# Performance work log

Measured on AMD Instinct MI355X. Metric: run time of the kernel, lower is better.

Reference implementation:

```python
import jax, jax.numpy as jnp
import numpy as np

B, S, HID = 2, 1024, 4096
NH, NKV, HD = 32, 8, 128
GROUPS = NH // NKV  # 4
BITS = 8
SCALING = HD ** -0.5


def quantize_lastdim(x, bits=BITS):
    """Asymmetric min-max fake-quant per row of the last dim (groupsize=-1),
    matching ActQuantizer.find_params + quantize/dequantize."""
    qmax = float(2 ** bits - 1)
    xmin = jnp.minimum(jnp.min(x, axis=-1, keepdims=True), 0.0)
    xmax = jnp.maximum(jnp.max(x, axis=-1, keepdims=True), 0.0)
    rng = xmax - xmin
    scale = jnp.where(rng == 0, 1.0, rng / qmax)
    zero = jnp.round(-xmin / scale)
    q = jnp.clip(jnp.round(x / scale) + zero, 0.0, qmax)
    return (q - zero) * scale


def rotate_half(x):
    x1, x2 = jnp.split(x, 2, axis=-1)
    return jnp.concatenate([-x2, x1], axis=-1)


def setup_inputs() -> dict:
    key = jax.random.key(0)
    ks = jax.random.split(key, 5)
    hidden_states = jax.random.normal(ks[0], (B, S, HID), dtype=jnp.float32)
    w_std = 0.02
    Wq = w_std * jax.random.normal(ks[1], (NH * HD, HID), dtype=jnp.float32)
    Wk = w_std * jax.random.normal(ks[2], (NKV * HD, HID), dtype=jnp.float32)
    Wv = w_std * jax.random.normal(ks[3], (NKV * HD, HID), dtype=jnp.float32)
    Wo = w_std * jax.random.normal(ks[4], (HID, NH * HD), dtype=jnp.float32)
    # RoPE tables (theta=10000)
    inv_freq = 1.0 / (10000.0 ** (jnp.arange(0, HD, 2, dtype=jnp.float32) / HD))
    freqs = jnp.outer(jnp.arange(S, dtype=jnp.float32), inv_freq)  # [S, HD/2]
    emb = jnp.concatenate([freqs, freqs], axis=-1)  # [S, HD]
    cos = jnp.broadcast_to(jnp.cos(emb)[None], (B, S, HD)).astype(jnp.float32)
    sin = jnp.broadcast_to(jnp.sin(emb)[None], (B, S, HD)).astype(jnp.float32)
    # additive causal mask [B,1,S,S]
    causal = jnp.tril(jnp.ones((S, S), dtype=bool))
    attention_mask = jnp.where(causal, 0.0, -1e9).astype(jnp.float32)
    attention_mask = jnp.broadcast_to(attention_mask[None, None], (B, 1, S, S))
    return {"hidden_states": hidden_states, "cos": cos, "sin": sin,
            "attention_mask": attention_mask, "Wq": Wq, "Wk": Wk, "Wv": Wv, "Wo": Wo}


def reference(hidden_states, cos, sin, attention_mask, Wq, Wk, Wv, Wo):
    b, s, _ = hidden_states.shape
    # projections -> [B, H, S, D]
    q = (hidden_states @ Wq.T).reshape(b, s, NH, HD).transpose(0, 2, 1, 3)
    k = (hidden_states @ Wk.T).reshape(b, s, NKV, HD).transpose(0, 2, 1, 3)
    v = (hidden_states @ Wv.T).reshape(b, s, NKV, HD).transpose(0, 2, 1, 3)
    # RoPE (HF: unsqueeze cos/sin at head dim)
    c = cos[:, None, :, :]
    si = sin[:, None, :, :]
    q = q * c + rotate_half(q) * si
    k = k * c + rotate_half(k) * si
    # SmoothK per-channel: subtract per-channel mean over the sequence
    # (softmax-invariant outlier smoothing of K before quantization)
    k = k - jnp.mean(k, axis=2, keepdims=True)
    # activation fake-quant of Q, K (per token over head_dim)
    q = quantize_lastdim(q)
    k = quantize_lastdim(k)
    # V quantized along the sequence axis (module transposes dims 2,3 first)
    v = quantize_lastdim(v.transpose(0, 1, 3, 2)).transpose(0, 1, 3, 2)
    # GQA repeat
    k_rep = jnp.repeat(k, GROUPS, axis=1)
    v_rep = jnp.repeat(v, GROUPS, axis=1)
    scores = jnp.einsum('bhqd,bhkd->bhqk', q, k_rep) * SCALING + attention_mask
    w = jax.nn.softmax(scores.astype(jnp.float32), axis=-1).astype(q.dtype)
    # fake-quant attention weights per row (groupsize=-1, so no padding)
    w = quantize_lastdim(w)
    attn = jnp.einsum('bhqk,bhkd->bhqd', w, v_rep)
    attn = attn.transpose(0, 2, 1, 3).reshape(b, s, NH * HD)
    out = attn @ Wo.T
    return (out, w)
```

## Files before the change

kernel.cpp:

```cpp
#include <hip/hip_runtime.h>
#include <math.h>
#include <stdint.h>

typedef unsigned int u32;
typedef unsigned short u16;
typedef __bf16 bf16x8 __attribute__((ext_vector_type(8)));
typedef float f32x4 __attribute__((ext_vector_type(4)));
typedef unsigned short u16x8 __attribute__((ext_vector_type(8)));
typedef unsigned short u16x4 __attribute__((ext_vector_type(4)));

constexpr int   Bb  = 2;
constexpr int   Ss  = 1024;
constexpr int   HID = 4096;
constexpr int   NH  = 32;
constexpr int   NKV = 8;
constexpr int   HD  = 128;
constexpr float SCALING = 0.0883883476483184405501f;

enum { M_QKV = 0, M_OUT = 3 };

__device__ __forceinline__ u16 f2bf(float f) {
  u32 u = __builtin_bit_cast(u32, f);
  u = u + 0x7fffu + ((u >> 16) & 1u);
  return (u16)(u >> 16);
}

__device__ __forceinline__ void gld_lds16(const void* g, void* l) {
  __builtin_amdgcn_global_load_lds(
      (const __attribute__((address_space(1))) u32*)(uintptr_t)g,
      (__attribute__((address_space(3))) u32*)(uintptr_t)l, 16, 0, 0);
}

template <int MODE>
__global__ __launch_bounds__(512) void mfma_gemm(
    const u16* __restrict__ Abf_g,
    const u16* __restrict__ B0, const u16* __restrict__ B1,
    const u16* __restrict__ B2,
    float* __restrict__ Cf, float* __restrict__ Ck, float* __restrict__ Cv,
    int K) {
  __shared__ u16 As[3][128 * 64];
  __shared__ u16 Bs[3][256 * 64];

  const int tid = threadIdx.x;
  const int lane = tid & 63;
  const int wid = tid >> 6;
  const int wr = wid >> 2;
  const int wc = wid & 3;
  const int fr = lane & 15;
  const int fq = lane >> 4;

  constexpr int GX = (MODE == M_QKV) ? 24 : 16;
  constexpr int CPX = (MODE == M_QKV) ? 48 : 32;
  const int bid = blockIdx.x;
  const int wg = (bid & 7) * CPX + (bid >> 3);
  const int bx = wg % GX;
  const int by = wg / GX;

  const int m0 = by * 128;
  int nloc = 0;

  const u16* Abf = Abf_g + (size_t)m0 * K;
  const u16* Bp = nullptr;
  int which = 0;

  if (MODE == M_QKV) {
    if (bx < 16)      { which = 0; Bp = B0 + (size_t)bx * 256 * K;        nloc = bx * 256; }
    else if (bx < 20) { which = 1; Bp = B1 + (size_t)(bx - 16) * 256 * K; nloc = (bx - 16) * 256; }
    else              { which = 2; Bp = B2 + (size_t)(bx - 20) * 256 * K; nloc = (bx - 20) * 256; }
  } else {
    Bp = B0 + (size_t)bx * 256 * K;
    nloc = bx * 256;
  }

  f32x4 acc[4][4];
#pragma unroll
  for (int i = 0; i < 4; i++)
#pragma unroll
    for (int j = 0; j < 4; j++) acc[i][j] = (f32x4){0.f, 0.f, 0.f, 0.f};

  const int arow0 = wr * 64 + wc * 16;
  const int brow0 = wc * 64 + wr * 32;
  const int sub8 = lane >> 3;
  const int sl8 = lane & 7;

  auto stageA = [&](int t, int s) {
    const int ko = t * 64;
#pragma unroll
    for (int g = 0; g < 2; ++g) {
      const int r0 = arow0 + g * 8;
      const int row = r0 + sub8;
      gld_lds16(Abf + (size_t)row * K + ko + ((sl8 ^ (row & 7)) * 8),
                &As[s][r0 * 64]);
    }
  };
  auto stageB2 = [&](int t, int s, int gbase) {
    const int ko = t * 64;
#pragma unroll
    for (int g = 0; g < 2; ++g) {
      const int r0 = brow0 + (gbase + g) * 8;
      const int row = r0 + sub8;
      gld_lds16(Bp + (size_t)row * K + ko + ((sl8 ^ (row & 7)) * 8),
                &Bs[s][r0 * 64]);
    }
  };

  const int nk = K >> 6;

  stageA(0, 0); stageB2(0, 0, 0); stageB2(0, 0, 2);
  stageA(1, 1); stageB2(1, 1, 0); stageB2(1, 1, 2);
  asm volatile("s_waitcnt vmcnt(6)" ::: "memory");
  __builtin_amdgcn_sched_barrier(0);
  __builtin_amdgcn_s_barrier();

  int buf = 0, nxt = 2;
  for (int kt = 0; kt < nk; ++kt) {
    const bool st = (kt + 2 < nk);

    {
      bf16x8 av[4], bv[4];
#pragma unroll
      for (int i = 0; i < 4; ++i) {
        const int r = wr * 64 + i * 16 + fr;
        av[i] = *(const bf16x8*)&As[buf][r * 64 + ((fq ^ (r & 7)) * 8)];
      }
#pragma unroll
      for (int j = 0; j < 4; ++j) {
        const int r = wc * 64 + j * 16 + fr;
        bv[j] = *(const bf16x8*)&Bs[buf][r * 64 + ((fq ^ (r & 7)) * 8)];
      }
      if (st) { stageA(kt + 2, nxt); stageB2(kt + 2, nxt, 0); }
      __builtin_amdgcn_s_barrier();
      asm volatile("s_waitcnt lgkmcnt(0)" ::: "memory");
      __builtin_amdgcn_sched_barrier(0);
      __builtin_amdgcn_s_setprio(1);
#pragma unroll
      for (int i = 0; i < 4; i++)
#pragma unroll
        for (int j = 0; j < 4; j++)
          acc[i][j] = __builtin_amdgcn_mfma_f32_16x16x32_bf16(av[i], bv[j], acc[i][j], 0, 0, 0);
      __builtin_amdgcn_s_setprio(0);
    }

    {
      bf16x8 av[4], bv[4];
#pragma unroll
      for (int i = 0; i < 4; ++i) {
        const int r = wr * 64 + i * 16 + fr;
        av[i] = *(const bf16x8*)&As[buf][r * 64 + (((4 + fq) ^ (r & 7)) * 8)];
      }
#pragma unroll
      for (int j = 0; j < 4; ++j) {
        const int r = wc * 64 + j * 16 + fr;
        bv[j] = *(const bf16x8*)&Bs[buf][r * 64 + (((4 + fq) ^ (r & 7)) * 8)];
      }
      if (st) { stageB2(kt + 2, nxt, 2); }
      __builtin_amdgcn_s_barrier();
      asm volatile("s_waitcnt lgkmcnt(0)" ::: "memory");
      __builtin_amdgcn_sched_barrier(0);
      __builtin_amdgcn_s_setprio(1);
#pragma unroll
      for (int i = 0; i < 4; i++)
#pragma unroll
        for (int j = 0; j < 4; j++)
          acc[i][j] = __builtin_amdgcn_mfma_f32_16x16x32_bf16(av[i], bv[j], acc[i][j], 0, 0, 0);
      __builtin_amdgcn_s_setprio(0);
    }

    if (st) {
      asm volatile("s_waitcnt vmcnt(6)" ::: "memory");
    } else {
      asm volatile("s_waitcnt vmcnt(0)" ::: "memory");
    }
    __builtin_amdgcn_sched_barrier(0);
    __builtin_amdgcn_s_barrier();
    buf = (buf == 2) ? 0 : buf + 1;
    nxt = (nxt == 2) ? 0 : nxt + 1;
  }

#pragma unroll
  for (int i = 0; i < 4; i++) {
#pragma unroll
    for (int j = 0; j < 4; j++) {
      const int n = nloc + wc * 64 + j * 16 + fr;
      const int mb = m0 + wr * 64 + i * 16 + fq * 4;
      if (MODE == M_QKV && which == 2) {
        const int b = mb >> 10, s = mb & 1023, h = n >> 7, d = n & 127;
        float4 v4 = {acc[i][j][0], acc[i][j][1], acc[i][j][2], acc[i][j][3]};
        *(float4*)&Cv[((size_t)(b * NKV + h) * HD + d) * Ss + s] = v4;
      } else {
#pragma unroll
        for (int e = 0; e < 4; e++) {
          const int m = mb + e;
          float val = acc[i][j][e];
          if (MODE == M_QKV) {
            const int b = m >> 10, s = m & 1023, h = n >> 7, d = n & 127;
            if (which == 0) Cf[((size_t)(b * NH + h) * Ss + s) * HD + d] = val;
            else            Ck[((size_t)(b * NKV + h) * Ss + s) * HD + d] = val;
          } else {
            Cf[(size_t)m * HID + n] = val;
          }
        }
      }
    }
  }
}

__global__ __launch_bounds__(512, 4) void fused_attn(
    const u16* __restrict__ qb,
    const u16* __restrict__ kb,
    const u16* __restrict__ vTb,
    float* __restrict__ wout,
    u16* __restrict__ attnb) {
  __shared__ u16 Ks[2][64 * 128];
  __shared__ u16 Vs[2][128 * 64];
  __shared__ float scl_l[8][16];

  const int a = 7 - (int)(blockIdx.x >> 6);
  const int bh = blockIdx.x & 63;
  const int b = bh >> 5, h = bh & 31;
  const int kv = h >> 2;
  const int tid = threadIdx.x;
  const int lane = tid & 63;
  const int wq = tid >> 6;
  const int fr = lane & 15, fq = lane >> 4;

  const int nt = 2 * a + 2;
  const int Q0 = a * 128;
  const int qw0 = Q0 + wq * 16;
  const int dband = qw0 >> 6;

  const u16* Kb = kb + (size_t)(b * NKV + kv) * Ss * HD;
  const u16* Vb = vTb + (size_t)(b * NKV + kv) * HD * Ss;
  float* wrow = wout + (size_t)bh * Ss * Ss;

  if (a < 7) {
    const int base = 64 * nt;
    const int n4 = (Ss - base) >> 2;
    const int row = Q0 + (tid >> 2);
    float4* wp = (float4*)&wrow[(size_t)row * Ss + base];
    for (int c = tid & 3; c < n4; c += 4) wp[c] = float4{0.f, 0.f, 0.f, 0.f};
  }

  auto stageK = [&](int t, int s) {
#pragma unroll
    for (int g = 0; g < 2; ++g) {
      const int c = wq * 2 + g;
      const int idx = c * 64 + lane;
      const int row = idx >> 4, sl = idx & 15;
      const int slot = sl ^ (row & 15);
      gld_lds16(Kb + (size_t)(t * 64 + row) * HD + slot * 8, &Ks[s][c * 512]);
    }
  };
  auto stageV = [&](int t, int s) {
#pragma unroll
    for (int g = 0; g < 2; ++g) {
      const int c = wq * 2 + g;
      const int idx = c * 64 + lane;
      const int d = idx >> 3, sl = idx & 7;
      const int slot = sl ^ (d & 7);
      gld_lds16(Vb + (size_t)d * Ss + t * 64 + slot * 8, &Vs[s][c * 512]);
    }
  };

  bf16x8 qf[4];
#pragma unroll
  for (int kk = 0; kk < 4; kk++)
    qf[kk] = *(const bf16x8*)&qb[((size_t)bh * Ss + qw0 + fr) * HD + kk * 32 + fq * 8];

  float m[4], l[4];
#pragma unroll
  for (int i = 0; i < 4; i++) { m[i] = -1e30f; l[i] = 0.f; }

  stageK(0, 0);
  for (int t = 0; t < nt; ++t) {
    if (t + 1 < nt) {
      stageK(t + 1, (t + 1) & 1);
      asm volatile("s_waitcnt vmcnt(2)" ::: "memory");
    } else {
      asm volatile("s_waitcnt vmcnt(0)" ::: "memory");
    }
    __builtin_amdgcn_sched_barrier(0);
    __builtin_amdgcn_s_barrier();
    const u16* Kt = &Ks[t & 1][0];

    f32x4 sa[4];
#pragma unroll
    for (int jn = 0; jn < 4; jn++) sa[jn] = (f32x4){0.f, 0.f, 0.f, 0.f};
#pragma unroll
    for (int kk = 0; kk < 4; ++kk) {
      bf16x8 kfv[4];
#pragma unroll
      for (int jn = 0; jn < 4; ++jn) {
        const int row = jn * 16 + fr;
        kfv[jn] = *(const bf16x8*)&Kt[row * 128 + (((kk * 4 + fq) ^ fr) * 8)];
      }
#pragma unroll
      for (int jn = 0; jn < 4; ++jn)
        sa[jn] = __builtin_amdgcn_mfma_f32_16x16x32_bf16(qf[kk], kfv[jn], sa[jn], 0, 0, 0);
    }

    const bool diag = (t >= dband);
#pragma unroll
    for (int e = 0; e < 4; ++e) {
      const int qrow = qw0 + fq * 4 + e;
      float sv[4];
      float rmax = -1e30f;
#pragma unroll
      for (int jn = 0; jn < 4; ++jn) {
        float s = sa[jn][e] * SCALING;
        if (diag && (t * 64 + jn * 16 + fr > qrow)) s = -1e30f;
        sv[jn] = s;
        rmax = fmaxf(rmax, s);
      }
#pragma unroll
      for (int o = 1; o < 16; o <<= 1) rmax = fmaxf(rmax, __shfl_xor(rmax, o));
      const float mn = fmaxf(m[e], rmax);
      const float cc = __expf(m[e] - mn);
      float rs = __expf(sv[0] - mn) + __expf(sv[1] - mn) +
                 __expf(sv[2] - mn) + __expf(sv[3] - mn);
#pragma unroll
      for (int o = 1; o < 16; o <<= 1) rs += __shfl_xor(rs, o);
      l[e] = l[e] * cc + rs;
      m[e] = mn;
    }
    __builtin_amdgcn_s_barrier();
  }

  float scl[4];
#pragma unroll
  for (int e = 0; e < 4; e++) scl[e] = 1.f / (255.f * l[e]);
  if (fr == 0) {
#pragma unroll
    for (int e = 0; e < 4; e++) scl_l[wq][fq * 4 + e] = scl[e];
  }

  f32x4 acc2[8];
#pragma unroll
  for (int j = 0; j < 8; j++) acc2[j] = (f32x4){0.f, 0.f, 0.f, 0.f};

  const int wrrow = lane >> 2, wrq = lane & 3;
  const float sclr = scl_l[wq][wrrow];

  stageK(0, 0);
  stageV(0, 0);
  for (int t = 0; t < nt; ++t) {
    if (t + 1 < nt) {
      stageK(t + 1, (t + 1) & 1);
      stageV(t + 1, (t + 1) & 1);
      asm volatile("s_waitcnt vmcnt(4)" ::: "memory");
    } else {
      asm volatile("s_waitcnt vmcnt(0)" ::: "memory");
    }
    __builtin_amdgcn_sched_barrier(0);
    __builtin_amdgcn_s_barrier();
    const u16* Kt = &Ks[t & 1][0];
    const u16* Vt = &Vs[t & 1][0];
    u16* pl = &Ks[t & 1][wq * 1024];

    f32x4 sa[4];
#pragma unroll
    for (int jn = 0; jn < 4; jn++) sa[jn] = (f32x4){0.f, 0.f, 0.f, 0.f};
#pragma unroll
    for (int kk = 0; kk < 4; ++kk) {
      bf16x8 kfv[4];
#pragma unroll
      for (int jn = 0; jn < 4; ++jn) {
        const int row = jn * 16 + fr;
        kfv[jn] = *(const bf16x8*)&Kt[row * 128 + (((kk * 4 + fq) ^ fr) * 8)];
      }
#pragma unroll
      for (int jn = 0; jn < 4; ++jn)
        sa[jn] = __builtin_amdgcn_mfma_f32_16x16x32_bf16(qf[kk], kfv[jn], sa[jn], 0, 0, 0);
    }
    __builtin_amdgcn_s_barrier();

    const bool diag = (t >= dband);
#pragma unroll
    for (int e = 0; e < 4; ++e) {
      const int qrow = qw0 + fq * 4 + e;
      const int r16 = fq * 4 + e;
#pragma unroll
      for (int jn = 0; jn < 4; ++jn) {
        const int kc = t * 64 + jn * 16 + fr;
        float qv = 0.f;
        if (!diag || kc <= qrow)
          qv = rintf(fminf(255.f * __expf(sa[jn][e] * SCALING - m[e]), 255.f));
        const int col = jn * 16 + fr;
        const int byte = r16 * 128 + (((col >> 3) ^ (r16 & 7)) * 16) + (col & 7) * 2;
        *(u16*)((char*)pl + byte) = f2bf(qv);
      }
    }

    {
      const int s0 = (2 * wrq) ^ (wrrow & 7);
      const int s1 = (2 * wrq + 1) ^ (wrrow & 7);
      bf16x8 p0 = *(const bf16x8*)((char*)pl + wrrow * 128 + s0 * 16);
      bf16x8 p1 = *(const bf16x8*)((char*)pl + wrrow * 128 + s1 * 16);
      float* wp = &wrow[(size_t)(qw0 + wrrow) * Ss + t * 64 + wrq * 16];
      float4 o0, o1, o2, o3;
      o0.x = (float)p0[0] * sclr; o0.y = (float)p0[1] * sclr;
      o0.z = (float)p0[2] * sclr; o0.w = (float)p0[3] * sclr;
      o1.x = (float)p0[4] * sclr; o1.y = (float)p0[5] * sclr;
      o1.z = (float)p0[6] * sclr; o1.w = (float)p0[7] * sclr;
      o2.x = (float)p1[0] * sclr; o2.y = (float)p1[1] * sclr;
      o2.z = (float)p1[2] * sclr; o2.w = (float)p1[3] * sclr;
      o3.x = (float)p1[4] * sclr; o3.y = (float)p1[5] * sclr;
      o3.z = (float)p1[6] * sclr; o3.w = (float)p1[7] * sclr;
      ((float4*)wp)[0] = o0; ((float4*)wp)[1] = o1;
      ((float4*)wp)[2] = o2; ((float4*)wp)[3] = o3;
    }

#pragma unroll
    for (int kk2 = 0; kk2 < 2; ++kk2) {
      const bf16x8 pa = *(const bf16x8*)((char*)pl + fr * 128 + (((kk2 * 4 + fq) ^ (fr & 7)) * 16));
#pragma unroll
      for (int jn2 = 0; jn2 < 8; ++jn2) {
        const int d = jn2 * 16 + fr;
        const bf16x8 vb = *(const bf16x8*)&Vt[d * 64 + (((kk2 * 4 + fq) ^ (d & 7)) * 8)];
        acc2[jn2] = __builtin_amdgcn_mfma_f32_16x16x32_bf16(pa, vb, acc2[jn2], 0, 0, 0);
      }
    }
    __builtin_amdgcn_s_barrier();
  }

#pragma unroll
  for (int e = 0; e < 4; ++e) {
    const int qrow = qw0 + fq * 4 + e;
#pragma unroll
    for (int jn2 = 0; jn2 < 8; ++jn2)
      attnb[((size_t)b * Ss + qrow) * HID + h * HD + jn2 * 16 + fr] =
          f2bf(acc2[jn2][e] * scl[e]);
  }
}

constexpr int CB_HS = Bb * Ss * HID / 2048;
constexpr int CB_WQ = NH * HD * HID / 2048;
constexpr int CB_WK = NKV * HD * HID / 2048;
constexpr int CB_WV = CB_WK;
constexpr int CB_WO = HID * NH * HD / 2048;

__global__ __launch_bounds__(256) void convert_all(
    const float* __restrict__ hs, const float* __restrict__ wq,
    const float* __restrict__ wk, const float* __restrict__ wv,
    const float* __restrict__ wo,
    u16* __restrict__ hsb, u16* __restrict__ wqb, u16* __restrict__ wkb,
    u16* __restrict__ wvb, u16* __restrict__ wob) {
  const int bid = blockIdx.x;
  const float* src;
  u16* dst;
  int base;
  if (bid < CB_HS) { src = hs; dst = hsb; base = 0; }
  else if (bid < CB_HS + CB_WQ) { src = wq; dst = wqb; base = CB_HS; }
  else if (bid < CB_HS + CB_WQ + CB_WK) { src = wk; dst = wkb; base = CB_HS + CB_WQ; }
  else if (bid < CB_HS + CB_WQ + CB_WK + CB_WV) { src = wv; dst = wvb; base = CB_HS + CB_WQ + CB_WK; }
  else { src = wo; dst = wob; base = CB_HS + CB_WQ + CB_WK + CB_WV; }
  const int i = (bid - base) * 256 + threadIdx.x;
  float4 a = ((const float4*)src)[2 * i];
  float4 b = ((const float4*)src)[2 * i + 1];
  u16x8 t;
  t[0] = f2bf(a.x); t[1] = f2bf(a.y); t[2] = f2bf(a.z); t[3] = f2bf(a.w);
  t[4] = f2bf(b.x); t[5] = f2bf(b.y); t[6] = f2bf(b.z); t[7] = f2bf(b.w);
  ((u16x8*)dst)[i] = t;
}

constexpr int PQ_Q = (Bb * NH * Ss) / 4;
constexpr int PQ_K = (Bb * NKV * Ss) / 4;
constexpr int PQ_V = Bb * NKV * HD;

__global__ __launch_bounds__(256) void postq(
    const float* __restrict__ q, u16* __restrict__ qb,
    float* __restrict__ k,
    const float* __restrict__ vT, u16* __restrict__ vTb,
    const float* __restrict__ cs, const float* __restrict__ sn) {
  const int bid = blockIdx.x;
  if (bid < PQ_Q) {
    const int row = bid * 4 + (threadIdx.x >> 6);
    const int lane = threadIdx.x & 63;
    const int s = row & (Ss - 1);
    const int b = row >> 15;
    const float* p = q + (size_t)row * HD;
    const float* cp = cs + ((size_t)b * Ss + s) * HD;
    const float* sp = sn + ((size_t)b * Ss + s) * HD;
    float x1 = p[lane], x2 = p[lane + 64];
    float r1 = x1 * cp[lane] - x2 * sp[lane];
    float r2 = x2 * cp[lane + 64] + x1 * sp[lane + 64];
    float mn = fminf(0.f, fminf(r1, r2));
    float mx = fmaxf(0.f, fmaxf(r1, r2));
#pragma unroll
    for (int o = 32; o; o >>= 1) {
      mn = fminf(mn, __shfl_xor(mn, o));
      mx = fmaxf(mx, __shfl_xor(mx, o));
    }
    float rng = mx - mn;
    float scale = (rng == 0.f) ? 1.f : rng / 255.f;
    float zero = rintf(-mn / scale);
    float q1 = fminf(fmaxf(rintf(r1 / scale) + zero, 0.f), 255.f);
    float q2 = fminf(fmaxf(rintf(r2 / scale) + zero, 0.f), 255.f);
    qb[(size_t)row * HD + lane] = f2bf((q1 - zero) * scale);
    qb[(size_t)row * HD + lane + 64] = f2bf((q2 - zero) * scale);
  } else if (bid < PQ_Q + PQ_K) {
    const int row = (bid - PQ_Q) * 4 + (threadIdx.x >> 6);
    const int lane = threadIdx.x & 63;
    const int s = row & (Ss - 1);
    const int b = row >> 13;
    float* p = k + (size_t)row * HD;
    const float* cp = cs + ((size_t)b * Ss + s) * HD;
    const float* sp = sn + ((size_t)b * Ss + s) * HD;
    float x1 = p[lane], x2 = p[lane + 64];
    float r1 = x1 * cp[lane] - x2 * sp[lane];
    float r2 = x2 * cp[lane + 64] + x1 * sp[lane + 64];
    p[lane] = r1;
    p[lane + 64] = r2;
  } else {
    const int vb = bid - PQ_Q - PQ_K;
    const float* p = vT + (size_t)vb * Ss;
    const int t = threadIdx.x;
    float4 x = ((const float4*)p)[t];
    float mn = fminf(0.f, fminf(fminf(x.x, x.y), fminf(x.z, x.w)));
    float mx = fmaxf(0.f, fmaxf(fmaxf(x.x, x.y), fmaxf(x.z, x.w)));
#pragma unroll
    for (int o = 32; o; o >>= 1) {
      mn = fminf(mn, __shfl_xor(mn, o));
      mx = fmaxf(mx, __shfl_xor(mx, o));
    }
    __shared__ float smn[4], smx[4];
    const int wid = t >> 6, lane = t & 63;
    if (lane == 0) { smn[wid] = mn; smx[wid] = mx; }
    __syncthreads();
    mn = fminf(fminf(smn[0], smn[1]), fminf(smn[2], smn[3]));
    mx = fmaxf(fmaxf(smx[0], smx[1]), fmaxf(smx[2], smx[3]));
    float rng = mx - mn;
    float scale = (rng == 0.f) ? 1.f : rng / 255.f;
    float zero = rintf(-mn / scale);
    u16x4 o4;
    o4[0] = f2bf((fminf(fmaxf(rintf(x.x / scale) + zero, 0.f), 255.f) - zero) * scale);
    o4[1] = f2bf((fminf(fmaxf(rintf(x.y / scale) + zero, 0.f), 255.f) - zero) * scale);
    o4[2] = f2bf((fminf(fmaxf(rintf(x.z / scale) + zero, 0.f), 255.f) - zero) * scale);
    o4[3] = f2bf((fminf(fmaxf(rintf(x.w / scale) + zero, 0.f), 255.f) - zero) * scale);
    ((u16x4*)vTb)[(size_t)vb * 256 + t] = o4;
  }
}

__global__ __launch_bounds__(1024) void kmean_kernel(const float* __restrict__ k,
                                                     float* __restrict__ kmean) {
  const int bh = blockIdx.x;
  const int d = threadIdx.x & 127;
  const int sl = threadIdx.x >> 7;
  const float* p = k + (size_t)bh * Ss * HD;
  float sum = 0.f;
  for (int s = sl; s < Ss; s += 8) sum += p[(size_t)s * HD + d];
  __shared__ float lds[8][128];
  lds[sl][d] = sum;
  __syncthreads();
  if (threadIdx.x < 128) {
    float t = 0.f;
#pragma unroll
    for (int i = 0; i < 8; i++) t += lds[i][threadIdx.x];
    kmean[bh * HD + threadIdx.x] = t * (1.f / 1024.f);
  }
}

__global__ __launch_bounds__(256) void k_subquant(const float* __restrict__ k,
                                                  u16* __restrict__ kb,
                                                  const float* __restrict__ kmean) {
  const int row = blockIdx.x * 4 + (threadIdx.x >> 6);
  const int lane = threadIdx.x & 63;
  const int bh = row >> 10;
  const float* p = k + (size_t)row * HD;
  float x1 = p[lane] - kmean[bh * HD + lane];
  float x2 = p[lane + 64] - kmean[bh * HD + lane + 64];
  float mn = fminf(0.f, fminf(x1, x2));
  float mx = fmaxf(0.f, fmaxf(x1, x2));
#pragma unroll
  for (int o = 32; o; o >>= 1) {
    mn = fminf(mn, __shfl_xor(mn, o));
    mx = fmaxf(mx, __shfl_xor(mx, o));
  }
  float rng = mx - mn;
  float scale = (rng == 0.f) ? 1.f : rng / 255.f;
  float zero = rintf(-mn / scale);
  float q1 = fminf(fmaxf(rintf(x1 / scale) + zero, 0.f), 255.f);
  float q2 = fminf(fmaxf(rintf(x2 / scale) + zero, 0.f), 255.f);
  kb[(size_t)row * HD + lane] = f2bf((q1 - zero) * scale);
  kb[(size_t)row * HD + lane + 64] = f2bf((q2 - zero) * scale);
}

extern "C" void kernel_launch(void* const* d_in, const int* in_sizes, int n_in,
                              void* d_out, int out_size, void* d_ws, size_t ws_size,
                              hipStream_t stream) {
  const float* hs = (const float*)d_in[0];
  const float* cosp = (const float*)d_in[1];
  const float* sinp = (const float*)d_in[2];
  const float* Wq = (const float*)d_in[4];
  const float* Wk = (const float*)d_in[5];
  const float* Wv = (const float*)d_in[6];
  const float* Wo = (const float*)d_in[7];

  float* out = (float*)d_out;
  float* wout = out + (size_t)Bb * Ss * HID;

  char* wsp = (char*)d_ws;
  auto alloc = [&](size_t bytes) {
    char* p = wsp;
    wsp += (bytes + 255) & ~(size_t)255;
    return p;
  };
  float* q     = (float*)alloc((size_t)Bb * NH * Ss * HD * 4);
  float* k     = (float*)alloc((size_t)Bb * NKV * Ss * HD * 4);
  float* vT    = (float*)alloc((size_t)Bb * NKV * Ss * HD * 4);
  float* kmean = (float*)alloc((size_t)Bb * NKV * HD * 4);
  u16* hsb = (u16*)alloc((size_t)Bb * Ss * HID * 2);
  u16* qb  = (u16*)alloc((size_t)Bb * NH * Ss * HD * 2);
  u16* kb  = (u16*)alloc((size_t)Bb * NKV * Ss * HD * 2);
  u16* vTb = (u16*)alloc((size_t)Bb * NKV * Ss * HD * 2);
  u16* Wqb = (u16*)alloc((size_t)NH * HD * HID * 2);
  u16* Wkb = (u16*)alloc((size_t)NKV * HD * HID * 2);
  u16* Wvb = (u16*)alloc((size_t)NKV * HD * HID * 2);
  u16* Wob = (u16*)alloc((size_t)HID * NH * HD * 2);
  u16* attnb = (u16*)q;

  convert_all<<<CB_HS + CB_WQ + CB_WK + CB_WV + CB_WO, 256, 0, stream>>>(
      hs, Wq, Wk, Wv, Wo, hsb, Wqb, Wkb, Wvb, Wob);

  mfma_gemm<M_QKV><<<dim3(384), 512, 0, stream>>>(
      hsb, Wqb, Wkb, Wvb, q, k, vT, HID);

  postq<<<PQ_Q + PQ_K + PQ_V, 256, 0, stream>>>(q, qb, k, vT, vTb, cosp, sinp);
  kmean_kernel<<<Bb * NKV, 1024, 0, stream>>>(k, kmean);
  k_subquant<<<(Bb * NKV * Ss) / 4, 256, 0, stream>>>(k, kb, kmean);

  fused_attn<<<dim3(512), 512, 0, stream>>>(qb, kb, vTb, wout, attnb);

  mfma_gemm<M_OUT><<<dim3(256), 512, 0, stream>>>(
      attnb, Wob, nullptr, nullptr, out, nullptr, nullptr, HID);
}
```

Baseline: 480.0 us.

## Shrink attention tiles to 64 query rows and drop GEMM block swizzle

```diff
diff --git a/kernel.cpp b/kernel.cpp
--- a/kernel.cpp
+++ b/kernel.cpp
@@ -49,14 +49,8 @@
   const int fr = lane & 15;
   const int fq = lane >> 4;
 
-  constexpr int GX = (MODE == M_QKV) ? 24 : 16;
-  constexpr int CPX = (MODE == M_QKV) ? 48 : 32;
-  const int bid = blockIdx.x;
-  const int wg = (bid & 7) * CPX + (bid >> 3);
-  const int bx = wg % GX;
-  const int by = wg / GX;
-
-  const int m0 = by * 128;
+  const int bx = blockIdx.x;
+  const int m0 = blockIdx.y * 128;
   int nloc = 0;
 
   const u16* Abf = Abf_g + (size_t)m0 * K;
@@ -205,7 +199,7 @@
   }
 }
 
-__global__ __launch_bounds__(512, 4) void fused_attn(
+__global__ __launch_bounds__(256) void fused_attn(
     const u16* __restrict__ qb,
     const u16* __restrict__ kb,
     const u16* __restrict__ vTb,
@@ -213,9 +207,10 @@
     u16* __restrict__ attnb) {
   __shared__ u16 Ks[2][64 * 128];
   __shared__ u16 Vs[2][128 * 64];
-  __shared__ float scl_l[8][16];
-
-  const int a = 7 - (int)(blockIdx.x >> 6);
+  __shared__ u16 plds[4][16 * 64];
+  __shared__ float scl_l[4][16];
+
+  const int a = 15 - (int)(blockIdx.x >> 6);
   const int bh = blockIdx.x & 63;
   const int b = bh >> 5, h = bh & 31;
   const int kv = h >> 2;
@@ -224,43 +219,47 @@
   const int wq = tid >> 6;
   const int fr = lane & 15, fq = lane >> 4;
 
-  const int nt = 2 * a + 2;
-  const int Q0 = a * 128;
+  const int nt = a + 1;
+  const int Q0 = a * 64;
   const int qw0 = Q0 + wq * 16;
-  const int dband = qw0 >> 6;
 
   const u16* Kb = kb + (size_t)(b * NKV + kv) * Ss * HD;
   const u16* Vb = vTb + (size_t)(b * NKV + kv) * HD * Ss;
   float* wrow = wout + (size_t)bh * Ss * Ss;
 
-  if (a < 7) {
-    const int base = 64 * nt;
-    const int n4 = (Ss - base) >> 2;
-    const int row = Q0 + (tid >> 2);
-    float4* wp = (float4*)&wrow[(size_t)row * Ss + base];
-    for (int c = tid & 3; c < n4; c += 4) wp[c] = float4{0.f, 0.f, 0.f, 0.f};
-  }
-
   auto stageK = [&](int t, int s) {
 #pragma unroll
-    for (int g = 0; g < 2; ++g) {
-      const int c = wq * 2 + g;
-      const int idx = c * 64 + lane;
+    for (int c = 0; c < 4; ++c) {
+      const int idx0 = (c * 4 + wq) * 64;
+      const int idx = idx0 + lane;
       const int row = idx >> 4, sl = idx & 15;
       const int slot = sl ^ (row & 15);
-      gld_lds16(Kb + (size_t)(t * 64 + row) * HD + slot * 8, &Ks[s][c * 512]);
+      gld_lds16(Kb + (size_t)(t * 64 + row) * HD + slot * 8, &Ks[s][idx0 * 8]);
     }
   };
   auto stageV = [&](int t, int s) {
 #pragma unroll
-    for (int g = 0; g < 2; ++g) {
-      const int c = wq * 2 + g;
-      const int idx = c * 64 + lane;
+    for (int c = 0; c < 4; ++c) {
+      const int idx0 = (c * 4 + wq) * 64;
+      const int idx = idx0 + lane;
       const int d = idx >> 3, sl = idx & 7;
       const int slot = sl ^ (d & 7);
-      gld_lds16(Vb + (size_t)d * Ss + t * 64 + slot * 8, &Vs[s][c * 512]);
+      gld_lds16(Vb + (size_t)d * Ss + t * 64 + slot * 8, &Vs[s][idx0 * 8]);
     }
   };
+
+  stageK(0, 0);
+
+  if (a < 15) {
+    const int base = 64 * nt;
+    const int n4 = 16 * (15 - a);
+#pragma unroll
+    for (int r0 = 0; r0 < 4; ++r0) {
+      const int row = Q0 + r0 * 16 + (tid >> 4);
+      float4* wp = (float4*)&wrow[(size_t)row * Ss + base];
+      for (int c = tid & 15; c < n4; c += 16) wp[c] = float4{0.f, 0.f, 0.f, 0.f};
+    }
+  }
 
   bf16x8 qf[4];
 #pragma unroll
@@ -271,11 +270,10 @@
 #pragma unroll
   for (int i = 0; i < 4; i++) { m[i] = -1e30f; l[i] = 0.f; }
 
-  stageK(0, 0);
   for (int t = 0; t < nt; ++t) {
     if (t + 1 < nt) {
       stageK(t + 1, (t + 1) & 1);
-      asm volatile("s_waitcnt vmcnt(2)" ::: "memory");
+      asm volatile("s_waitcnt vmcnt(4)" ::: "memory");
     } else {
       asm volatile("s_waitcnt vmcnt(0)" ::: "memory");
     }
@@ -299,7 +297,7 @@
         sa[jn] = __builtin_amdgcn_mfma_f32_16x16x32_bf16(qf[kk], kfv[jn], sa[jn], 0, 0, 0);
     }
 
-    const bool diag = (t >= dband);
+    const bool diag = (t == a);
 #pragma unroll
     for (int e = 0; e < 4; ++e) {
       const int qrow = qw0 + fq * 4 + e;
@@ -338,6 +336,7 @@
 #pragma unroll
   for (int j = 0; j < 8; j++) acc2[j] = (f32x4){0.f, 0.f, 0.f, 0.f};
 
+  u16* pl = &plds[wq][0];
   const int wrrow = lane >> 2, wrq = lane & 3;
   const float sclr = scl_l[wq][wrrow];
 
@@ -347,7 +346,7 @@
     if (t + 1 < nt) {
       stageK(t + 1, (t + 1) & 1);
       stageV(t + 1, (t + 1) & 1);
-      asm volatile("s_waitcnt vmcnt(4)" ::: "memory");
+      asm volatile("s_waitcnt vmcnt(8)" ::: "memory");
     } else {
       asm volatile("s_waitcnt vmcnt(0)" ::: "memory");
     }
@@ -355,7 +354,6 @@
     __builtin_amdgcn_s_barrier();
     const u16* Kt = &Ks[t & 1][0];
     const u16* Vt = &Vs[t & 1][0];
-    u16* pl = &Ks[t & 1][wq * 1024];
 
     f32x4 sa[4];
 #pragma unroll
@@ -372,9 +370,8 @@
       for (int jn = 0; jn < 4; ++jn)
         sa[jn] = __builtin_amdgcn_mfma_f32_16x16x32_bf16(qf[kk], kfv[jn], sa[jn], 0, 0, 0);
     }
-    __builtin_amdgcn_s_barrier();
-
-    const bool diag = (t >= dband);
+
+    const bool diag = (t == a);
 #pragma unroll
     for (int e = 0; e < 4; ++e) {
       const int qrow = qw0 + fq * 4 + e;
@@ -622,15 +619,15 @@
   convert_all<<<CB_HS + CB_WQ + CB_WK + CB_WV + CB_WO, 256, 0, stream>>>(
       hs, Wq, Wk, Wv, Wo, hsb, Wqb, Wkb, Wvb, Wob);
 
-  mfma_gemm<M_QKV><<<dim3(384), 512, 0, stream>>>(
+  mfma_gemm<M_QKV><<<dim3(24, 16), 512, 0, stream>>>(
       hsb, Wqb, Wkb, Wvb, q, k, vT, HID);
 
   postq<<<PQ_Q + PQ_K + PQ_V, 256, 0, stream>>>(q, qb, k, vT, vTb, cosp, sinp);
   kmean_kernel<<<Bb * NKV, 1024, 0, stream>>>(k, kmean);
   k_subquant<<<(Bb * NKV * Ss) / 4, 256, 0, stream>>>(k, kb, kmean);
 
-  fused_attn<<<dim3(512), 512, 0, stream>>>(qb, kb, vTb, wout, attnb);
-
-  mfma_gemm<M_OUT><<<dim3(256), 512, 0, stream>>>(
+  fused_attn<<<dim3(1024), 256, 0, stream>>>(qb, kb, vTb, wout, attnb);
+
+  mfma_gemm<M_OUT><<<dim3(16, 16), 512, 0, stream>>>(
       attnb, Wob, nullptr, nullptr, out, nullptr, nullptr, HID);
 }
```

Result: faster. 423.8 us (-11.7%).
